# Kernel optimization log

Measured on AMD Instinct MI355X. Metric: run time of the kernel, lower is better.

Reference implementation:

```python
import jax, jax.numpy as jnp
import numpy as np

EPS = 1e-5
NEG_SLOPE = 0.2


def _minmax(a):
    m = jnp.min(a)
    return (a - m) / (jnp.max(a) - m)


def _bn(x2d, gamma, beta):
    # train-mode BatchNorm1d: stats over axis 0 (biased variance)
    mu = x2d.mean(0)
    var = x2d.var(0)
    return gamma * (x2d - mu) * jax.lax.rsqrt(var + EPS) + beta


def _leaky(a):
    return jnp.where(a >= 0, a, NEG_SLOPE * a)


def setup_inputs() -> dict:
    key = jax.random.key(0)
    ks = jax.random.split(key, 10)
    B, C, N = 256, 1024, 80
    stdv = 1.0 / np.sqrt(C)
    return {
        "x": jax.random.normal(ks[0], (B, C, N), jnp.float32),
        "out1": jax.random.normal(ks[1], (B, N), jnp.float32),
        "adj_param": jax.random.uniform(ks[2], (N, N), jnp.float32),
        "static_weight": jax.random.uniform(ks[3], (C, C), jnp.float32, -stdv, stdv),
        "dynamic_weight": jax.random.uniform(ks[4], (C, C), jnp.float32, -stdv, stdv),
        "conv_global_w": jax.random.normal(ks[5], (C, C), jnp.float32) * 0.02,
        "conv_global_b": jnp.zeros((C,), jnp.float32),
        "conv_co_w": jax.random.normal(ks[6], (N, 2 * C), jnp.float32) * 0.02,
        "conv_co_b": jnp.zeros((N,), jnp.float32),
        "bn_gamma": jnp.ones((C,), jnp.float32),
        "bn_beta": jnp.zeros((C,), jnp.float32),
        "bng_gamma": jnp.ones((C,), jnp.float32),
        "bng_beta": jnp.zeros((C,), jnp.float32),
    }


def reference(x, out1, adj_param, static_weight, dynamic_weight,
              conv_global_w, conv_global_b, conv_co_w, conv_co_b,
              bn_gamma, bn_beta, bng_gamma, bng_beta):
    B, C, N = x.shape

    # ---- static GCN ----
    sadj = _minmax(adj_param)                               # (N,N)
    D = jax.lax.rsqrt(sadj.sum(1))                          # A.sum(1)^-0.5
    adj = D[:, None] * sadj.T * D[None, :]                  # gen_adj, diag matmuls as broadcast
    support = jnp.einsum('bcn,co->bno', x, static_weight)   # (B,N,C)
    h = jnp.einsum('nm,bmo->bno', adj, support)             # (B,N,C)
    h = _bn(h.reshape(-1, C), bn_gamma, bn_beta).reshape(B, N, C)
    out_static = _leaky(h).transpose(0, 2, 1)               # (B,C,N)
    x2 = x + out_static

    # ---- dynamic graph construction ----
    glb = x2.mean(2)                                        # GAP over nodes -> (B,C)
    glb = glb @ conv_global_w.T + conv_global_b             # 1x1 conv
    glb = _leaky(_bn(glb, bng_gamma, bng_beta))             # BN over batch (L=1)
    cat = jnp.concatenate([jnp.broadcast_to(glb[:, :, None], (B, C, N)), x2], axis=1)  # (B,2C,N)
    dadj = jnp.einsum('oc,bcn->bon', conv_co_w, cat) + conv_co_b[None, :, None]        # (B,N,N)
    dadj = _minmax(dadj)

    # ---- adjacency loss ----
    t1 = jnp.einsum('bn,bnm->bm', out1, dadj) / N
    loss = jnp.sum(jnp.linalg.norm(out1 - t1, axis=1))
    loss = loss + jnp.sum(jnp.linalg.norm((dadj - sadj).reshape(B, -1), axis=1))

    # ---- dynamic GCN ----
    Dd = jax.lax.rsqrt(dadj.sum(2))                         # (B,N)
    tadj = Dd[:, :, None] * dadj.transpose(0, 2, 1) * Dd[:, None, :]
    sup = jnp.einsum('bcn,co->bno', x2, dynamic_weight)
    h2 = jnp.einsum('bnm,bmo->bno', tadj, sup)
    h2 = _bn(h2.reshape(-1, C), bn_gamma, bn_beta).reshape(B, N, C).transpose(0, 2, 1)
    h2 = _leaky(h2)                                         # (B,C,N)
    return h2, loss
```

## Files before the change

kernel.cpp:

```cpp
#include <hip/hip_runtime.h>
#include <hip/hip_bf16.h>
#include <math.h>

#define TPB 256

constexpr int   B_  = 256;
constexpr int   C_  = 1024;
constexpr int   N_  = 80;
constexpr int   BNr = B_ * N_;
constexpr int   CN  = C_ * N_;
constexpr long  BCN = (long)B_ * C_ * N_;
constexpr int   NN  = N_ * N_;
constexpr int   BNN = B_ * NN;
constexpr float EPSf = 1e-5f;

typedef __bf16 bf16x8 __attribute__((ext_vector_type(8)));
typedef float  f32x4  __attribute__((ext_vector_type(4)));

__device__ __forceinline__ float leakyf(float v) { return v >= 0.0f ? v : 0.2f * v; }

__device__ __forceinline__ ushort f2bf(float f) {
  __hip_bfloat16 h = __float2bfloat16(f);
  ushort u; __builtin_memcpy(&u, &h, 2); return u;
}
__device__ __forceinline__ float b2f(ushort u) {
  __hip_bfloat16 h; __builtin_memcpy(&h, &u, 2);
  return __bfloat162float(h);
}

#define GLOBAL_AS __attribute__((address_space(1)))
#define LDS_AS    __attribute__((address_space(3)))
__device__ __forceinline__ void load_lds16(const void* g, void* l) {
  __builtin_amdgcn_global_load_lds((const GLOBAL_AS void*)g, (LDS_AS void*)l, 16, 0, 0);
}

__global__ __launch_bounds__(256) void k_prep_all(
    const float* __restrict__ Ws, const float* __restrict__ Wd,
    const float* __restrict__ Wco, const float* __restrict__ Wg,
    ushort* __restrict__ Wts, ushort* __restrict__ Wtd,
    ushort* __restrict__ Wco1t, ushort* __restrict__ Wco2t, ushort* __restrict__ Wg_bf,
    float* __restrict__ zbase,
    const float* __restrict__ ap, float* __restrict__ sadj,
    ushort* __restrict__ adj_bf, float* __restrict__ lossa) {
  __shared__ float sh[NN];
  __shared__ float red[TPB];
  __shared__ float sD[N_];
  __shared__ float s_lo, s_hi;
  const int t = threadIdx.x;
  const int blk = blockIdx.x;
  if (blk < 2048) {
    const float* W = (blk < 1024) ? Ws : Wd;
    ushort* Wt = (blk < 1024) ? Wts : Wtd;
    const int bb = blk & 1023;
    const int bx = bb & 31, by = bb >> 5;
    const int tx = t % 32, ty = t / 32;
    const int r0 = by * 32, c0 = bx * 32;
#pragma unroll
    for (int k = 0; k < 4; ++k) sh[(ty + 8 * k) * 33 + tx] = W[(size_t)(r0 + ty + 8 * k) * C_ + c0 + tx];
    __syncthreads();
#pragma unroll
    for (int k = 0; k < 4; ++k) Wt[(size_t)(c0 + ty + 8 * k) * C_ + r0 + tx] = f2bf(sh[tx * 33 + ty + 8 * k]);
  } else if (blk < 2208) {
    const int i4 = ((blk - 2048) * TPB + t) * 4;
    const int o = i4 >> 11, k = i4 & 2047;
    float4 v = *(const float4*)&Wco[(size_t)o * 2048 + k];
    ushort4 u;
    u.x = f2bf(v.x); u.y = f2bf(v.y); u.z = f2bf(v.z); u.w = f2bf(v.w);
    if (k < C_) *(ushort4*)&Wco1t[(size_t)o * C_ + k] = u;
    else        *(ushort4*)&Wco2t[(size_t)o * C_ + (k - C_)] = u;
  } else if (blk < 3232) {
    const long i4 = ((long)(blk - 2208) * TPB + t) * 4;
    float4 v = *(const float4*)&Wg[i4];
    ushort4 u;
    u.x = f2bf(v.x); u.y = f2bf(v.y); u.z = f2bf(v.z); u.w = f2bf(v.w);
    *(ushort4*)&Wg_bf[i4] = u;
  } else if (blk < 3256) {
    const int i = ((blk - 3232) * TPB + t) * 4;
    float4 z = make_float4(0.f, 0.f, 0.f, 0.f);
    *(float4*)&zbase[i] = z;
  } else {
    float lo = 3.4e38f, hi = -3.4e38f;
    for (int i = t; i < NN; i += TPB) { float v = ap[i]; sh[i] = v; lo = fminf(lo, v); hi = fmaxf(hi, v); }
    red[t] = lo; __syncthreads();
    for (int o = 128; o > 0; o >>= 1) { if (t < o) red[t] = fminf(red[t], red[t + o]); __syncthreads(); }
    if (t == 0) s_lo = red[0];
    __syncthreads();
    red[t] = hi; __syncthreads();
    for (int o = 128; o > 0; o >>= 1) { if (t < o) red[t] = fmaxf(red[t], red[t + o]); __syncthreads(); }
    if (t == 0) s_hi = red[0];
    __syncthreads();
    const float inv = 1.0f / (s_hi - s_lo);
    for (int i = t; i < NN; i += TPB) { float v = (sh[i] - s_lo) * inv; sh[i] = v; sadj[i] = v; }
    __syncthreads();
    if (t < N_) { float sum = 0.f; for (int m = 0; m < N_; ++m) sum += sh[t * N_ + m]; sD[t] = rsqrtf(sum); }
    if (t == 0) *lossa = 0.0f;
    __syncthreads();
    for (int i = t; i < N_ * 96; i += TPB) {
      const int n = i / 96, m = i % 96;
      adj_bf[i] = f2bf((m < N_) ? sD[n] * sh[m * N_ + n] * sD[m] : 0.0f);
    }
  }
}

__global__ __launch_bounds__(256) void k_fold_mfma(const float* __restrict__ Xf32,
                                                   const ushort* __restrict__ Xbf,
                                                   const void* __restrict__ adjsrc,
                                                   ushort* __restrict__ outp, int mode,
                                                   const float* __restrict__ dmm) {
  __shared__ __align__(16) ushort sX[128][104];
  __shared__ __align__(16) ushort sAdj[80][104];
  __shared__ float sD[N_];
  const int t = threadIdx.x;
  const int b  = blockIdx.x >> 3;
  const int c0 = (blockIdx.x & 7) * 128;

  if (mode == 0) {
    const ushort* ab = (const ushort*)adjsrc;
    for (int i = t; i < (N_ * 96) / 4; i += TPB) {
      ushort4 v = *(const ushort4*)&ab[i * 4];
      *(ushort4*)&sAdj[(i * 4) / 96][(i * 4) % 96] = v;
    }
    __syncthreads();
  } else {
    float* sF = (float*)&sX[0][0];
    const float* db = (const float*)adjsrc + (size_t)b * NN;
    const float lo = dmm[0], inv = dmm[1];
    for (int i = t; i < NN / 4; i += TPB) {
      float4 v = *(const float4*)&db[i * 4];
      v.x = (v.x - lo) * inv; v.y = (v.y - lo) * inv;
      v.z = (v.z - lo) * inv; v.w = (v.w - lo) * inv;
      *(float4*)&sF[i * 4] = v;
    }
    __syncthreads();
    if (t < N_) { float s = 0.f; for (int m = 0; m < N_; ++m) s += sF[t * N_ + m]; sD[t] = rsqrtf(s); }
    __syncthreads();
    for (int i = t; i < N_ * 96; i += TPB) {
      const int n = i / 96, m = i % 96;
      sAdj[n][m] = f2bf((m < N_) ? sF[m * N_ + n] * sD[n] * sD[m] : 0.0f);
    }
    __syncthreads();
  }

  if (mode == 0) {
    const float* Xb = Xf32 + ((size_t)b * C_ + c0) * N_;
    for (int i = t; i < (128 * N_) / 4; i += TPB) {
      float4 v = *(const float4*)&Xb[i * 4];
      const int r = (i * 4) / N_, m = (i * 4) % N_;
      ushort4 u; u.x = f2bf(v.x); u.y = f2bf(v.y); u.z = f2bf(v.z); u.w = f2bf(v.w);
      *(ushort4*)&sX[r][m] = u;
    }
  } else {
    const ushort* Xb = Xbf + ((size_t)b * C_ + c0) * N_;
    for (int i = t; i < (128 * N_) / 8; i += TPB) {
      const int r = i / 10, m = (i % 10) * 8;
      uint4 v = *(const uint4*)&Xb[(size_t)r * N_ + m];
      *(uint4*)&sX[r][m] = v;
    }
  }
  for (int i = t; i < (128 * 16) / 4; i += TPB) {
    const int r = i / 4, m = 80 + (i % 4) * 4;
    ushort4 z; z.x = 0; z.y = 0; z.z = 0; z.w = 0;
    *(ushort4*)&sX[r][m] = z;
  }
  __syncthreads();

  const int lane = t & 63, wid = t >> 6;
  const int l16 = lane & 15, lq = lane >> 4;
  f32x4 acc[2][5];
#pragma unroll
  for (int i = 0; i < 2; ++i)
#pragma unroll
    for (int j = 0; j < 5; ++j) { f32x4 z = {0.f, 0.f, 0.f, 0.f}; acc[i][j] = z; }
  bf16x8 af[2][3], bfr[5][3];
#pragma unroll
  for (int i = 0; i < 2; ++i)
#pragma unroll
    for (int kk = 0; kk < 3; ++kk)
      af[i][kk] = *(const bf16x8*)&sX[wid * 32 + i * 16 + l16][kk * 32 + lq * 8];
#pragma unroll
  for (int j = 0; j < 5; ++j)
#pragma unroll
    for (int kk = 0; kk < 3; ++kk)
      bfr[j][kk] = *(const bf16x8*)&sAdj[j * 16 + l16][kk * 32 + lq * 8];
#pragma unroll
  for (int i = 0; i < 2; ++i)
#pragma unroll
    for (int j = 0; j < 5; ++j)
#pragma unroll
      for (int kk = 0; kk < 3; ++kk)
        acc[i][j] = __builtin_amdgcn_mfma_f32_16x16x32_bf16(af[i][kk], bfr[j][kk], acc[i][j], 0, 0, 0);

  ushort* ob = outp + (size_t)b * CN;
#pragma unroll
  for (int i = 0; i < 2; ++i) {
    const int c = c0 + wid * 32 + i * 16 + lq * 4;
#pragma unroll
    for (int j = 0; j < 5; ++j) {
      const int n = j * 16 + l16;
      ushort4 u;
      u.x = f2bf(acc[i][j][0]); u.y = f2bf(acc[i][j][1]);
      u.z = f2bf(acc[i][j][2]); u.w = f2bf(acc[i][j][3]);
      *(ushort4*)&ob[(size_t)n * C_ + c] = u;
    }
  }
}

__global__ __launch_bounds__(512, 2) void k_gemm_256(const ushort* __restrict__ A,
                                                     const ushort* __restrict__ Bt,
                                                     void* __restrict__ outp, int out_bf,
                                                     float* __restrict__ bnsum,
                                                     float* __restrict__ bnsq) {
  __shared__ ushort sA[2][256 * 64];
  __shared__ ushort sB[2][256 * 64];
  const int t = threadIdx.x;
  const int lane = t & 63, wid = t >> 6;
  const int wm = wid >> 2, wn = wid & 3;
  const int l16 = lane & 15, lq = lane >> 4;

  const int lin = blockIdx.x;
  const int xcd = lin & 7, bi = lin >> 3;
  const int tm = xcd * 10 + (bi >> 2);
  const int tn = bi & 3;
  const int m0 = tm * 256, o0 = tn * 256;

  const int srow = t >> 3;
  const int sswz = ((t & 7) ^ ((t >> 3) & 7)) * 8;

  f32x4 acc[8][4];
#pragma unroll
  for (int i = 0; i < 8; ++i)
#pragma unroll
    for (int j = 0; j < 4; ++j) { f32x4 z = {0.f, 0.f, 0.f, 0.f}; acc[i][j] = z; }

  bf16x8 afr[4][2], bfr0[2][2], bfr1[2][2];

#define STA(PAR, ROWB, KT) load_lds16(A  + (size_t)(m0 + (ROWB) + srow) * C_ + (KT) * 64 + sswz, \
                                      &sA[PAR][((ROWB) + (wid << 3)) * 64])
#define STB(PAR, ROWB, KT) load_lds16(Bt + (size_t)(o0 + (ROWB) + srow) * C_ + (KT) * 64 + sswz, \
                                      &sB[PAR][((ROWB) + (wid << 3)) * 64])
#define STA_H(PAR, H, KT) { STA(PAR, (H)*128, KT); STA(PAR, (H)*128 + 64, KT); }
#define STB_H(PAR, H, KT) { STB(PAR, (H)*128, KT); STB(PAR, (H)*128 + 64, KT); }

#define RDA(PAR, MH)                                                                      \
  _Pragma("unroll") for (int fi = 0; fi < 4; ++fi) {                                      \
    const int row = ((MH) ? 128 : 0) + wm * 64 + fi * 16 + l16;                           \
    _Pragma("unroll") for (int kk = 0; kk < 2; ++kk)                                      \
      afr[fi][kk] = *(const bf16x8*)&sA[PAR][row * 64 + ((kk * 4 + lq) ^ (l16 & 7)) * 8]; \
  }
#define RDB(PAR, NH, DST)                                                                 \
  _Pragma("unroll") for (int gi = 0; gi < 2; ++gi) {                                      \
    const int row = ((NH) ? 128 : 0) + wn * 32 + gi * 16 + l16;                           \
    _Pragma("unroll") for (int kk = 0; kk < 2; ++kk)                                      \
      DST[gi][kk] = *(const bf16x8*)&sB[PAR][row * 64 + ((kk * 4 + lq) ^ (l16 & 7)) * 8]; \
  }

#define MFMAS(MH, NH, BF)                                                          \
  _Pragma("unroll") for (int kk = 0; kk < 2; ++kk)                                 \
  _Pragma("unroll") for (int fi = 0; fi < 4; ++fi)                                 \
  _Pragma("unroll") for (int gi = 0; gi < 2; ++gi)                                 \
    acc[(MH) * 4 + fi][(NH) * 2 + gi] = __builtin_amdgcn_mfma_f32_16x16x32_bf16(   \
        afr[fi][kk], BF[gi][kk], acc[(MH) * 4 + fi][(NH) * 2 + gi], 0, 0, 0);

#define PHASE(MH, NH, BF, RD, STAGES, VMW)                                         \
  {                                                                                \
    RD                                                                             \
    STAGES                                                                         \
    asm volatile("s_barrier" ::: "memory");                                        \
    asm volatile("s_waitcnt lgkmcnt(0)" ::: "memory");                             \
    __builtin_amdgcn_s_setprio(1);                                                 \
    MFMAS(MH, NH, BF)                                                              \
    __builtin_amdgcn_s_setprio(0);                                                 \
    VMW                                                                            \
    asm volatile("s_barrier" ::: "memory");                                        \
  }

  STA_H(0, 0, 0); STA_H(0, 1, 0); STB_H(0, 0, 0); STB_H(0, 1, 0);
  STA_H(1, 0, 1); STB_H(1, 1, 1);
  asm volatile("s_waitcnt vmcnt(4)" ::: "memory");
  asm volatile("s_barrier" ::: "memory");

  for (int i = 0; i < 7; ++i) {
    const int t1 = 2 * i + 1, t2 = 2 * i + 2, t3 = 2 * i + 3;
    PHASE(0, 0, bfr0, RDA(0, 0) RDB(0, 0, bfr0), { STA_H(1, 1, t1); }, {})
    PHASE(0, 1, bfr1, RDB(0, 1, bfr1),           { STB_H(1, 0, t1); }, {})
    PHASE(1, 1, bfr1, RDA(0, 1),                 { STA_H(0, 0, t2); }, {})
    PHASE(1, 0, bfr0, {},                        { STB_H(0, 1, t2); }, { asm volatile("s_waitcnt vmcnt(4)" ::: "memory"); })
    PHASE(0, 0, bfr0, RDA(1, 0) RDB(1, 0, bfr0), { STA_H(0, 1, t2); }, {})
    PHASE(0, 1, bfr1, RDB(1, 1, bfr1),           { STB_H(0, 0, t2); }, {})
    PHASE(1, 1, bfr1, RDA(1, 1),                 { STA_H(1, 0, t3); }, {})
    PHASE(1, 0, bfr0, {},                        { STB_H(1, 1, t3); }, { asm volatile("s_waitcnt vmcnt(4)" ::: "memory"); })
  }
  PHASE(0, 0, bfr0, RDA(0, 0) RDB(0, 0, bfr0), { STA_H(1, 1, 15); }, {})
  PHASE(0, 1, bfr1, RDB(0, 1, bfr1),           { STB_H(1, 0, 15); }, {})
  PHASE(1, 1, bfr1, RDA(0, 1),                 {}, {})
  PHASE(1, 0, bfr0, {},                        {}, { asm volatile("s_waitcnt vmcnt(0)" ::: "memory"); })
  PHASE(0, 0, bfr0, RDA(1, 0) RDB(1, 0, bfr0), {}, {})
  PHASE(0, 1, bfr1, RDB(1, 1, bfr1),           {}, {})
  PHASE(1, 1, bfr1, RDA(1, 1),                 {}, {})
  PHASE(1, 0, bfr0, {},                        {}, {})

#pragma unroll
  for (int f = 0; f < 8; ++f) {
    const int gmb = (f < 4) ? (wm * 64 + f * 16) : (128 + wm * 64 + (f - 4) * 16);
    const int mg = m0 + gmb + lq * 4;
    const int b  = mg / 80;
    const int n0 = mg - b * 80;
#pragma unroll
    for (int gi = 0; gi < 4; ++gi) {
      const int gnb = (gi < 2) ? (wn * 32 + gi * 16) : (128 + wn * 32 + (gi - 2) * 16);
      const int og = o0 + gnb + l16;
      const size_t off = (size_t)b * CN + (size_t)og * N_ + n0;
      if (out_bf) {
        ushort4 u;
        u.x = f2bf(acc[f][gi][0]); u.y = f2bf(acc[f][gi][1]);
        u.z = f2bf(acc[f][gi][2]); u.w = f2bf(acc[f][gi][3]);
        *(ushort4*)((ushort*)outp + off) = u;
      } else {
        *(f32x4*)((float*)outp + off) = acc[f][gi];
      }
    }
  }

  {
    float* redS = (float*)&sA[0][0];
    float* redQ = redS + 2048;
    const int slot = wm * 4 + lq;
#pragma unroll
    for (int gi = 0; gi < 4; ++gi) {
      float s = 0.f, q = 0.f;
#pragma unroll
      for (int f = 0; f < 8; ++f)
#pragma unroll
        for (int r = 0; r < 4; ++r) { const float v = acc[f][gi][r]; s += v; q += v * v; }
      const int gnb = (gi < 2) ? (wn * 32 + gi * 16) : (128 + wn * 32 + (gi - 2) * 16);
      const int ol = gnb + l16;
      redS[ol * 8 + slot] = s;
      redQ[ol * 8 + slot] = q;
    }
    __syncthreads();
    if (t < 256) {
      float s = 0.f, q = 0.f;
#pragma unroll
      for (int k = 0; k < 8; ++k) { s += redS[t * 8 + k]; q += redQ[t * 8 + k]; }
      atomicAdd(&bnsum[o0 + t], s);
      atomicAdd(&bnsq[o0 + t], q);
    }
  }
#undef STA
#undef STB
#undef STA_H
#undef STB_H
#undef RDA
#undef RDB
#undef MFMAS
#undef PHASE
}

__global__ __launch_bounds__(256) void k_dadj_mfma(const ushort* __restrict__ A,
                                                   const ushort* __restrict__ Bw,
                                                   const float* __restrict__ go,
                                                   const float* __restrict__ bco,
                                                   float* __restrict__ dadj,
                                                   float* __restrict__ bmin,
                                                   float* __restrict__ bmax) {
  __shared__ ushort smA[128 * 32];
  __shared__ ushort smB[80 * 32];
  const int t = threadIdx.x;
  const int lane = t & 63, wid = t >> 6;
  const int m0 = blockIdx.x * 128;
  const int rto = t >> 2, ch = t & 3;
  const size_t gA0 = (size_t)(m0 + rto) * C_ + (size_t)ch * 8;
  ushort* ldsA = smA + wid * 512;
  const int l16 = lane & 15, lq = lane >> 4;
  const int wrow = wid * 32;
  f32x4 zero = {0.f, 0.f, 0.f, 0.f};
  f32x4 acc[2][5];
#pragma unroll
  for (int i = 0; i < 2; ++i)
#pragma unroll
    for (int j = 0; j < 5; ++j) acc[i][j] = zero;
  for (int k0 = 0; k0 < C_; k0 += 32) {
    load_lds16(A + gA0 + k0,            ldsA);
    load_lds16(A + gA0 + 64 * C_ + k0,  ldsA + 2048);
    {
      const int idx = t;
      uint4 v = *(const uint4*)&Bw[(size_t)(idx >> 2) * C_ + k0 + (idx & 3) * 8];
      *(uint4*)&smB[idx * 8] = v;
      if (t < 64) {
        const int idx2 = 256 + t;
        uint4 v2 = *(const uint4*)&Bw[(size_t)(idx2 >> 2) * C_ + k0 + (idx2 & 3) * 8];
        *(uint4*)&smB[idx2 * 8] = v2;
      }
    }
    __syncthreads();
    bf16x8 af[2], bfr[5];
#pragma unroll
    for (int i = 0; i < 2; ++i) af[i]  = *(const bf16x8*)&smA[(wrow + i * 16 + l16) * 32 + lq * 8];
#pragma unroll
    for (int j = 0; j < 5; ++j) bfr[j] = *(const bf16x8*)&smB[(j * 16 + l16) * 32 + lq * 8];
#pragma unroll
    for (int i = 0; i < 2; ++i)
#pragma unroll
      for (int j = 0; j < 5; ++j)
        acc[i][j] = __builtin_amdgcn_mfma_f32_16x16x32_bf16(af[i], bfr[j], acc[i][j], 0, 0, 0);
    __syncthreads();
  }
  float vlo = 3.4e38f, vhi = -3.4e38f;
#pragma unroll
  for (int i = 0; i < 2; ++i) {
    const int mg = m0 + wrow + i * 16 + lq * 4;
    const int b  = mg / 80;
    const int n0 = mg - b * 80;
    const float* gob = go + b * N_;
#pragma unroll
    for (int j = 0; j < 5; ++j) {
      const int o = j * 16 + l16;
      const float g = gob[o] + bco[o];
      f32x4 v = acc[i][j];
      v[0] += g; v[1] += g; v[2] += g; v[3] += g;
      vlo = fminf(vlo, fminf(fminf(v[0], v[1]), fminf(v[2], v[3])));
      vhi = fmaxf(vhi, fmaxf(fmaxf(v[0], v[1]), fmaxf(v[2], v[3])));
      *(f32x4*)&dadj[(size_t)b * NN + (size_t)o * N_ + n0] = v;
    }
  }
  float* red = (float*)smA;
  red[t] = vlo; red[TPB + t] = vhi;
  __syncthreads();
  for (int o = 128; o > 0; o >>= 1) {
    if (t < o) {
      red[t] = fminf(red[t], red[t + o]);
      red[TPB + t] = fmaxf(red[TPB + t], red[TPB + t + o]);
    }
    __syncthreads();
  }
  if (t == 0) { bmin[blockIdx.x] = red[0]; bmax[blockIdx.x] = red[TPB]; }
}

__global__ __launch_bounds__(256) void k_glb_mfma(const ushort* __restrict__ A,
                                                  const ushort* __restrict__ Bw,
                                                  const float* __restrict__ bias,
                                                  float* __restrict__ outp) {
  __shared__ ushort smA[2][64 * 32];
  __shared__ ushort smB[2][64 * 32];
  const int t = threadIdx.x;
  const int lane = t & 63, wid = t >> 6;
  const int o0 = blockIdx.x * 64, m0 = blockIdx.y * 64;
  const int rto = t >> 2, ch = t & 3;
  const size_t gA0 = (size_t)(m0 + rto) * C_ + (size_t)ch * 8;
  const size_t gB0 = (size_t)(o0 + rto) * C_ + (size_t)ch * 8;
  const int l16 = lane & 15, lq = lane >> 4;
  const int wm = wid & 1, wn = wid >> 1;
  f32x4 zero = {0.f, 0.f, 0.f, 0.f};
  f32x4 acc[2][2];
#pragma unroll
  for (int i = 0; i < 2; ++i)
#pragma unroll
    for (int j = 0; j < 2; ++j) acc[i][j] = zero;
  for (int k0 = 0; k0 < C_; k0 += 64) {
    load_lds16(A  + gA0 + k0,       smA[0] + wid * 512);
    load_lds16(A  + gA0 + k0 + 32,  smA[1] + wid * 512);
    load_lds16(Bw + gB0 + k0,       smB[0] + wid * 512);
    load_lds16(Bw + gB0 + k0 + 32,  smB[1] + wid * 512);
    __syncthreads();
#pragma unroll
    for (int h = 0; h < 2; ++h) {
      bf16x8 af[2], bfr[2];
#pragma unroll
      for (int i = 0; i < 2; ++i) af[i]  = *(const bf16x8*)&smA[h][(wm * 32 + i * 16 + l16) * 32 + lq * 8];
#pragma unroll
      for (int j = 0; j < 2; ++j) bfr[j] = *(const bf16x8*)&smB[h][(wn * 32 + j * 16 + l16) * 32 + lq * 8];
#pragma unroll
      for (int i = 0; i < 2; ++i)
#pragma unroll
        for (int j = 0; j < 2; ++j)
          acc[i][j] = __builtin_amdgcn_mfma_f32_16x16x32_bf16(af[i], bfr[j], acc[i][j], 0, 0, 0);
    }
    __syncthreads();
  }
#pragma unroll
  for (int i = 0; i < 2; ++i) {
    const int mg = m0 + wm * 32 + i * 16 + lq * 4;
#pragma unroll
    for (int j = 0; j < 2; ++j) {
      const int og = o0 + wn * 32 + j * 16 + l16;
      const float bs = bias[og];
      f32x4 v = acc[i][j];
#pragma unroll
      for (int r = 0; r < 4; ++r) outp[(size_t)(mg + r) * C_ + og] = v[r] + bs;
    }
  }
}

__global__ __launch_bounds__(256) void k_go_mfma(const ushort* __restrict__ A,
                                                 const ushort* __restrict__ Bw,
                                                 float* __restrict__ go) {
  __shared__ ushort smA[128 * 32];
  __shared__ ushort smB[80 * 32];
  const int t = threadIdx.x;
  const int lane = t & 63, wid = t >> 6;
  const int kbase = blockIdx.x * 128;
  const int m0 = blockIdx.y * 128;
  const int rto = t >> 2, ch = t & 3;
  const size_t gA0 = (size_t)(m0 + rto) * C_ + (size_t)ch * 8;
  ushort* ldsA = smA + wid * 512;
  const int l16 = lane & 15, lq = lane >> 4;
  const int wrow = wid * 32;
  f32x4 zero = {0.f, 0.f, 0.f, 0.f};
  f32x4 acc[2][5];
#pragma unroll
  for (int i = 0; i < 2; ++i)
#pragma unroll
    for (int j = 0; j < 5; ++j) acc[i][j] = zero;
  for (int kk0 = 0; kk0 < 128; kk0 += 32) {
    const int k0 = kbase + kk0;
    load_lds16(A + gA0 + k0,            ldsA);
    load_lds16(A + gA0 + 64 * C_ + k0,  ldsA + 2048);
    {
      const int idx = t;
      uint4 v = *(const uint4*)&Bw[(size_t)(idx >> 2) * C_ + k0 + (idx & 3) * 8];
      *(uint4*)&smB[idx * 8] = v;
      if (t < 64) {
        const int idx2 = 256 + t;
        uint4 v2 = *(const uint4*)&Bw[(size_t)(idx2 >> 2) * C_ + k0 + (idx2 & 3) * 8];
        *(uint4*)&smB[idx2 * 8] = v2;
      }
    }
    __syncthreads();
    bf16x8 af[2], bfr[5];
#pragma unroll
    for (int i = 0; i < 2; ++i) af[i]  = *(const bf16x8*)&smA[(wrow + i * 16 + l16) * 32 + lq * 8];
#pragma unroll
    for (int j = 0; j < 5; ++j) bfr[j] = *(const bf16x8*)&smB[(j * 16 + l16) * 32 + lq * 8];
#pragma unroll
    for (int i = 0; i < 2; ++i)
#pragma unroll
      for (int j = 0; j < 5; ++j)
        acc[i][j] = __builtin_amdgcn_mfma_f32_16x16x32_bf16(af[i], bfr[j], acc[i][j], 0, 0, 0);
    __syncthreads();
  }
#pragma unroll
  for (int i = 0; i < 2; ++i) {
    const int mg = m0 + wrow + i * 16 + lq * 4;
#pragma unroll
    for (int j = 0; j < 5; ++j) {
      const int o = j * 16 + l16;
#pragma unroll
      for (int r = 0; r < 4; ++r)
        atomicAdd(&go[(size_t)(mg + r) * N_ + o], acc[i][j][r]);
    }
  }
}

__global__ __launch_bounds__(256) void k_x2_fused(
    const float* __restrict__ x, ushort* __restrict__ hx,
    const float* __restrict__ g, const float* __restrict__ be,
    const float* __restrict__ ssum, const float* __restrict__ ssq,
    ushort* __restrict__ x2t, ushort* __restrict__ glb0b) {
  __shared__ float s[64][84];
  __shared__ float pg[64], pm[64], pb[64];
  const int t = threadIdx.x;
  const long row0 = (long)blockIdx.x * 64;
  const int b = (int)(row0 >> 10), c0 = (int)(row0 & 1023);
  if (t < 64) {
    const int c = c0 + t;
    const float mu = ssum[c] * (1.0f / BNr);
    const float var = ssq[c] * (1.0f / BNr) - mu * mu;
    const float rstd = rsqrtf(var + EPSf);
    pg[t] = g[c] * rstd; pm[t] = mu; pb[t] = be[c];
  }
  __syncthreads();
  const float* xb = x  + row0 * N_;
  ushort*      hb = hx + row0 * N_;
  for (int i4 = t; i4 < (64 * N_) / 4; i4 += TPB) {
    const int e = i4 * 4, r = e / N_, n = e % N_;
    float4 xv = *(const float4*)&xb[e];
    ushort4 hu = *(const ushort4*)&hb[e];
    const float gm = pg[r], m = pm[r], bb = pb[r];
    float4 o;
    o.x = xv.x + leakyf(gm * (b2f(hu.x) - m) + bb);
    o.y = xv.y + leakyf(gm * (b2f(hu.y) - m) + bb);
    o.z = xv.z + leakyf(gm * (b2f(hu.z) - m) + bb);
    o.w = xv.w + leakyf(gm * (b2f(hu.w) - m) + bb);
    *(float4*)&s[r][n] = o;
    ushort4 ou;
    ou.x = f2bf(o.x); ou.y = f2bf(o.y); ou.z = f2bf(o.z); ou.w = f2bf(o.w);
    *(ushort4*)&hb[e] = ou;
  }
  __syncthreads();
  const int tx = t % 16, ty = t / 16;
  ushort* tb = x2t + (size_t)b * CN + c0 + tx * 4;
#pragma unroll
  for (int u = 0; u < 5; ++u) {
    const int n = ty + 16 * u;
    ushort4 v;
    v.x = f2bf(s[tx * 4 + 0][n]); v.y = f2bf(s[tx * 4 + 1][n]);
    v.z = f2bf(s[tx * 4 + 2][n]); v.w = f2bf(s[tx * 4 + 3][n]);
    *(ushort4*)&tb[(size_t)n * C_] = v;
  }
  {
    const int r = t >> 2, q = t & 3;
    float sacc = 0.f;
    for (int n = q; n < N_; n += 4) sacc += s[r][n];
    sacc += __shfl_down(sacc, 1);
    sacc += __shfl_down(sacc, 2);
    if (q == 0) glb0b[(size_t)b * C_ + c0 + r] = f2bf(sacc * (1.0f / N_));
  }
}

__global__ void k_bng(const float* __restrict__ glb1, const float* __restrict__ gg,
                      const float* __restrict__ gb, ushort* __restrict__ glbf) {
  const int c = blockIdx.x, t = threadIdx.x;
  const float v = glb1[(long)t * C_ + c];
  __shared__ float rs[TPB], rq[TPB];
  rs[t] = v; rq[t] = v * v; __syncthreads();
  for (int o = 128; o > 0; o >>= 1) { if (t < o) { rs[t] += rs[t + o]; rq[t] += rq[t + o]; } __syncthreads(); }
  __shared__ float sm, sr;
  if (t == 0) { const float m = rs[0] / B_; const float var = rq[0] / B_ - m * m; sm = m; sr = rsqrtf(var + EPSf); }
  __syncthreads();
  glbf[(long)t * C_ + c] = f2bf(leakyf(gg[c] * (v - sm) * sr + gb[c]));
}

__global__ void k_minmax2(const float* __restrict__ bmin, const float* __restrict__ bmax, float* __restrict__ dmm) {
  const int t = threadIdx.x;
  float lo = (t < 160) ? bmin[t] : 3.4e38f;
  float hi = (t < 160) ? bmax[t] : -3.4e38f;
  __shared__ float rl[TPB], rh[TPB];
  rl[t] = lo; rh[t] = hi; __syncthreads();
  for (int o = 128; o > 0; o >>= 1) { if (t < o) { rl[t] = fminf(rl[t], rl[t + o]); rh[t] = fmaxf(rh[t], rh[t + o]); } __syncthreads(); }
  if (t == 0) { dmm[0] = rl[0]; dmm[1] = 1.0f / (rh[0] - rl[0]); }
}

__global__ void k_loss(const float* __restrict__ dadj, const float* __restrict__ sadj,
                       const float* __restrict__ out1, float* __restrict__ lossa,
                       const float* __restrict__ dmm) {
  const int b = blockIdx.x, t = threadIdx.x;
  const float* db = dadj + (long)b * NN;
  const float* o1 = out1 + b * N_;
  const float lo = dmm[0], inv = dmm[1];
  float p2 = 0.f;
  for (int i = t; i < NN; i += TPB) { const float d = (db[i] - lo) * inv - sadj[i]; p2 += d * d; }
  float p1 = 0.f;
  if (t < N_) {
    float acc = 0.f;
    for (int n = 0; n < N_; ++n) acc += o1[n] * ((db[n * N_ + t] - lo) * inv);
    const float d = o1[t] - acc * (1.0f / N_);
    p1 = d * d;
  }
  __shared__ float red[TPB];
  __shared__ float s2;
  red[t] = p2; __syncthreads();
  for (int o = 128; o > 0; o >>= 1) { if (t < o) red[t] += red[t + o]; __syncthreads(); }
  if (t == 0) s2 = red[0];
  __syncthreads();
  red[t] = p1; __syncthreads();
  for (int o = 128; o > 0; o >>= 1) { if (t < o) red[t] += red[t + o]; __syncthreads(); }
  if (t == 0) atomicAdd(lossa, sqrtf(s2) + sqrtf(red[0]));
}

__global__ void k_final(const ushort* __restrict__ h2, float* __restrict__ outp,
                        const float* __restrict__ g, const float* __restrict__ be,
                        const float* __restrict__ ssum, const float* __restrict__ ssq,
                        const float* __restrict__ lossa) {
  const long i = ((long)blockIdx.x * TPB + threadIdx.x) * 4;
  const int c = (int)((i / N_) % C_);
  ushort4 hu = *(const ushort4*)&h2[i];
  const float mu = ssum[c] * (1.0f / BNr);
  const float rstd = rsqrtf(ssq[c] * (1.0f / BNr) - mu * mu + EPSf);
  const float gm = g[c] * rstd, bb = be[c];
  float4 v;
  v.x = leakyf(gm * (b2f(hu.x) - mu) + bb);
  v.y = leakyf(gm * (b2f(hu.y) - mu) + bb);
  v.z = leakyf(gm * (b2f(hu.z) - mu) + bb);
  v.w = leakyf(gm * (b2f(hu.w) - mu) + bb);
  *(float4*)&outp[i] = v;
  if (blockIdx.x == 0 && threadIdx.x == 0) outp[BCN] = *lossa;
}

extern "C" void kernel_launch(void* const* d_in, const int* in_sizes, int n_in,
                              void* d_out, int out_size, void* d_ws, size_t ws_size,
                              hipStream_t stream) {
  const float* x    = (const float*)d_in[0];
  const float* out1 = (const float*)d_in[1];
  const float* ap   = (const float*)d_in[2];
  const float* Ws   = (const float*)d_in[3];
  const float* Wd   = (const float*)d_in[4];
  const float* Wg   = (const float*)d_in[5];
  const float* bg   = (const float*)d_in[6];
  const float* Wco  = (const float*)d_in[7];
  const float* bco  = (const float*)d_in[8];
  const float* bn_g  = (const float*)d_in[9];
  const float* bn_b  = (const float*)d_in[10];
  const float* bng_g = (const float*)d_in[11];
  const float* bng_b = (const float*)d_in[12];
  float* out = (float*)d_out;

  float* w = (float*)d_ws;
  float* sadj  = w;
  float* dadj  = sadj + NN;
  float* glb0  = dadj + BNN;
  float* glb1  = glb0 + B_ * C_;
  float* glbf  = glb1 + B_ * C_;
  float* go    = glbf + B_ * C_;
  float* ssum1 = go + BNr;
  float* ssq1  = ssum1 + C_;
  float* ssum2 = ssq1 + C_;
  float* ssq2  = ssum2 + C_;
  float* bmin  = ssq2 + C_;
  float* bmax  = bmin + 512;
  float* dmm   = bmax + 512;
  float* lossa = dmm + 2;
  ushort* ub   = (ushort*)(((uintptr_t)(lossa + 1) + 255) & ~(uintptr_t)255);
  ushort* xa_bf  = ub;
  ushort* hT_bf  = xa_bf + BCN;
  ushort* Wts    = hT_bf + BCN;
  ushort* Wtd    = Wts + (size_t)C_ * C_;
  ushort* Wco2t  = Wtd + (size_t)C_ * C_;
  ushort* adj_bf = Wco2t + (size_t)N_ * C_;
  ushort* Wg_bf   = (ushort*)dadj;
  ushort* Wco1t   = (ushort*)dadj + (size_t)C_ * C_;
  ushort* glb0_bf = (ushort*)glb0;
  ushort* glbf_bf = (ushort*)glbf;
  ushort* x2t_bf  = xa_bf;

  k_prep_all<<<3257, TPB, 0, stream>>>(Ws, Wd, Wco, Wg, Wts, Wtd, Wco1t, Wco2t, Wg_bf,
                                       go, ap, sadj, adj_bf, lossa);

  k_fold_mfma<<<B_ * 8, TPB, 0, stream>>>(x, hT_bf, adj_bf, xa_bf, 0, dmm);
  k_gemm_256<<<320, 512, 0, stream>>>(xa_bf, Wts, hT_bf, 1, ssum1, ssq1);
  k_x2_fused<<<(B_ * C_) / 64, TPB, 0, stream>>>(x, hT_bf, bn_g, bn_b, ssum1, ssq1,
                                                 x2t_bf, glb0_bf);

  k_glb_mfma<<<dim3(C_ / 64, B_ / 64), TPB, 0, stream>>>(glb0_bf, Wg_bf, bg, glb1);
  k_bng<<<C_, TPB, 0, stream>>>(glb1, bng_g, bng_b, glbf_bf);
  k_go_mfma<<<dim3(8, B_ / 128), TPB, 0, stream>>>(glbf_bf, Wco1t, go);
  k_dadj_mfma<<<BNr / 128, TPB, 0, stream>>>(x2t_bf, Wco2t, go, bco, dadj, bmin, bmax);
  k_minmax2<<<1, TPB, 0, stream>>>(bmin, bmax, dmm);

  k_loss<<<B_, TPB, 0, stream>>>(dadj, sadj, out1, lossa, dmm);

  k_fold_mfma<<<B_ * 8, TPB, 0, stream>>>(x, hT_bf, dadj, xa_bf, 1, dmm);
  k_gemm_256<<<320, 512, 0, stream>>>(xa_bf, Wtd, hT_bf, 1, ssum2, ssq2);
  k_final<<<(int)(BCN / (4 * TPB)), TPB, 0, stream>>>(hT_bf, out, bn_g, bn_b, ssum2, ssq2, lossa);
}
```

Before: 503.4 us.

## Fuse BN-global stats into glb GEMM and fold minmax reduction into consumers

The global-branch BatchNorm statistics are now accumulated with atomics in the epilogue of the glb GEMM, and the normalize, leaky and bf16 conversion is applied while the go GEMM loads its A operand. This removes the separate k_bng kernel and the glbf buffer. The single-block min/max kernel is also removed: k_loss and k_fold_mfma each reduce the 160 per-block partials themselves. Two launches and a round trip through global memory go away, at the cost of redundant small reductions in every consumer block and atomics on two more zeroed buffers.

```diff
diff --git a/kernel.cpp b/kernel.cpp
--- a/kernel.cpp
+++ b/kernel.cpp
@@ -74,7 +74,7 @@
     ushort4 u;
     u.x = f2bf(v.x); u.y = f2bf(v.y); u.z = f2bf(v.z); u.w = f2bf(v.w);
     *(ushort4*)&Wg_bf[i4] = u;
-  } else if (blk < 3256) {
+  } else if (blk < 3258) {
     const int i = ((blk - 3232) * TPB + t) * 4;
     float4 z = make_float4(0.f, 0.f, 0.f, 0.f);
     *(float4*)&zbase[i] = z;
@@ -106,10 +106,13 @@
                                                    const ushort* __restrict__ Xbf,
                                                    const void* __restrict__ adjsrc,
                                                    ushort* __restrict__ outp, int mode,
-                                                   const float* __restrict__ dmm) {
+                                                   const float* __restrict__ bmin,
+                                                   const float* __restrict__ bmax) {
   __shared__ __align__(16) ushort sX[128][104];
   __shared__ __align__(16) ushort sAdj[80][104];
   __shared__ float sD[N_];
+  __shared__ float rl[TPB], rh[TPB];
+  __shared__ float s_lo, s_inv;
   const int t = threadIdx.x;
   const int b  = blockIdx.x >> 3;
   const int c0 = (blockIdx.x & 7) * 128;
@@ -122,9 +125,18 @@
     }
     __syncthreads();
   } else {
+    rl[t] = (t < 160) ? bmin[t] : 3.4e38f;
+    rh[t] = (t < 160) ? bmax[t] : -3.4e38f;
+    __syncthreads();
+    for (int o = 128; o > 0; o >>= 1) {
+      if (t < o) { rl[t] = fminf(rl[t], rl[t + o]); rh[t] = fmaxf(rh[t], rh[t + o]); }
+      __syncthreads();
+    }
+    if (t == 0) { s_lo = rl[0]; s_inv = 1.0f / (rh[0] - rl[0]); }
+    __syncthreads();
+    const float lo = s_lo, inv = s_inv;
     float* sF = (float*)&sX[0][0];
     const float* db = (const float*)adjsrc + (size_t)b * NN;
-    const float lo = dmm[0], inv = dmm[1];
     for (int i = t; i < NN / 4; i += TPB) {
       float4 v = *(const float4*)&db[i * 4];
       v.x = (v.x - lo) * inv; v.y = (v.y - lo) * inv;
@@ -439,7 +451,9 @@
 __global__ __launch_bounds__(256) void k_glb_mfma(const ushort* __restrict__ A,
                                                   const ushort* __restrict__ Bw,
                                                   const float* __restrict__ bias,
-                                                  float* __restrict__ outp) {
+                                                  float* __restrict__ outp,
+                                                  float* __restrict__ gsum,
+                                                  float* __restrict__ gsq) {
   __shared__ ushort smA[2][64 * 32];
   __shared__ ushort smB[2][64 * 32];
   const int t = threadIdx.x;
@@ -477,6 +491,7 @@
     }
     __syncthreads();
   }
+  float ssv[2] = {0.f, 0.f}, sqv[2] = {0.f, 0.f};
 #pragma unroll
   for (int i = 0; i < 2; ++i) {
     const int mg = m0 + wm * 32 + i * 16 + lq * 4;
@@ -486,25 +501,57 @@
       const float bs = bias[og];
       f32x4 v = acc[i][j];
 #pragma unroll
-      for (int r = 0; r < 4; ++r) outp[(size_t)(mg + r) * C_ + og] = v[r] + bs;
-    }
-  }
-}
-
-__global__ __launch_bounds__(256) void k_go_mfma(const ushort* __restrict__ A,
+      for (int r = 0; r < 4; ++r) {
+        const float val = v[r] + bs;
+        outp[(size_t)(mg + r) * C_ + og] = val;
+        ssv[j] += val; sqv[j] += val * val;
+      }
+    }
+  }
+  {
+    float* redS = (float*)&smA[0][0];
+    float* redQ = redS + 512;
+    const int slot = wm * 4 + lq;
+#pragma unroll
+    for (int j = 0; j < 2; ++j) {
+      const int ol = wn * 32 + j * 16 + l16;
+      redS[ol * 8 + slot] = ssv[j];
+      redQ[ol * 8 + slot] = sqv[j];
+    }
+    __syncthreads();
+    if (t < 64) {
+      float s = 0.f, q = 0.f;
+#pragma unroll
+      for (int k = 0; k < 8; ++k) { s += redS[t * 8 + k]; q += redQ[t * 8 + k]; }
+      atomicAdd(&gsum[o0 + t], s);
+      atomicAdd(&gsq[o0 + t], q);
+    }
+  }
+}
+
+__global__ __launch_bounds__(256) void k_go_mfma(const float* __restrict__ glb1,
                                                  const ushort* __restrict__ Bw,
+                                                 const float* __restrict__ gsum,
+                                                 const float* __restrict__ gsq,
+                                                 const float* __restrict__ gg,
+                                                 const float* __restrict__ gb,
                                                  float* __restrict__ go) {
   __shared__ ushort smA[128 * 32];
   __shared__ ushort smB[80 * 32];
+  __shared__ float pgm[C_], pmu[C_], pgb[C_];
   const int t = threadIdx.x;
   const int lane = t & 63, wid = t >> 6;
   const int kbase = blockIdx.x * 128;
   const int m0 = blockIdx.y * 128;
   const int rto = t >> 2, ch = t & 3;
-  const size_t gA0 = (size_t)(m0 + rto) * C_ + (size_t)ch * 8;
-  ushort* ldsA = smA + wid * 512;
   const int l16 = lane & 15, lq = lane >> 4;
   const int wrow = wid * 32;
+  for (int c = t; c < C_; c += TPB) {
+    const float mu = gsum[c] * (1.0f / B_);
+    const float var = gsq[c] * (1.0f / B_) - mu * mu;
+    pgm[c] = gg[c] * rsqrtf(var + EPSf); pmu[c] = mu; pgb[c] = gb[c];
+  }
+  __syncthreads();
   f32x4 zero = {0.f, 0.f, 0.f, 0.f};
   f32x4 acc[2][5];
 #pragma unroll
@@ -513,8 +560,25 @@
     for (int j = 0; j < 5; ++j) acc[i][j] = zero;
   for (int kk0 = 0; kk0 < 128; kk0 += 32) {
     const int k0 = kbase + kk0;
-    load_lds16(A + gA0 + k0,            ldsA);
-    load_lds16(A + gA0 + 64 * C_ + k0,  ldsA + 2048);
+#pragma unroll
+    for (int h = 0; h < 2; ++h) {
+      const float* src = &glb1[(size_t)(m0 + h * 64 + rto) * C_ + k0 + ch * 8];
+      float4 a0 = *(const float4*)src;
+      float4 a1 = *(const float4*)(src + 4);
+      float av[8] = {a0.x, a0.y, a0.z, a0.w, a1.x, a1.y, a1.z, a1.w};
+      ushort4 u0, u1;
+      const int cb = k0 + ch * 8;
+      u0.x = f2bf(leakyf(pgm[cb+0]*(av[0]-pmu[cb+0])+pgb[cb+0]));
+      u0.y = f2bf(leakyf(pgm[cb+1]*(av[1]-pmu[cb+1])+pgb[cb+1]));
+      u0.z = f2bf(leakyf(pgm[cb+2]*(av[2]-pmu[cb+2])+pgb[cb+2]));
+      u0.w = f2bf(leakyf(pgm[cb+3]*(av[3]-pmu[cb+3])+pgb[cb+3]));
+      u1.x = f2bf(leakyf(pgm[cb+4]*(av[4]-pmu[cb+4])+pgb[cb+4]));
+      u1.y = f2bf(leakyf(pgm[cb+5]*(av[5]-pmu[cb+5])+pgb[cb+5]));
+      u1.z = f2bf(leakyf(pgm[cb+6]*(av[6]-pmu[cb+6])+pgb[cb+6]));
+      u1.w = f2bf(leakyf(pgm[cb+7]*(av[7]-pmu[cb+7])+pgb[cb+7]));
+      *(ushort4*)&smA[h * 2048 + t * 8]     = u0;
+      *(ushort4*)&smA[h * 2048 + t * 8 + 4] = u1;
+    }
     {
       const int idx = t;
       uint4 v = *(const uint4*)&Bw[(size_t)(idx >> 2) * C_ + k0 + (idx & 3) * 8];
@@ -556,7 +620,7 @@
     const float* __restrict__ g, const float* __restrict__ be,
     const float* __restrict__ ssum, const float* __restrict__ ssq,
     ushort* __restrict__ x2t, ushort* __restrict__ glb0b) {
-  __shared__ float s[64][84];
+  __shared__ float s[64][85];
   __shared__ float pg[64], pm[64], pb[64];
   const int t = threadIdx.x;
   const long row0 = (long)blockIdx.x * 64;
@@ -607,36 +671,24 @@
   }
 }
 
-__global__ void k_bng(const float* __restrict__ glb1, const float* __restrict__ gg,
-                      const float* __restrict__ gb, ushort* __restrict__ glbf) {
-  const int c = blockIdx.x, t = threadIdx.x;
-  const float v = glb1[(long)t * C_ + c];
-  __shared__ float rs[TPB], rq[TPB];
-  rs[t] = v; rq[t] = v * v; __syncthreads();
-  for (int o = 128; o > 0; o >>= 1) { if (t < o) { rs[t] += rs[t + o]; rq[t] += rq[t + o]; } __syncthreads(); }
-  __shared__ float sm, sr;
-  if (t == 0) { const float m = rs[0] / B_; const float var = rq[0] / B_ - m * m; sm = m; sr = rsqrtf(var + EPSf); }
-  __syncthreads();
-  glbf[(long)t * C_ + c] = f2bf(leakyf(gg[c] * (v - sm) * sr + gb[c]));
-}
-
-__global__ void k_minmax2(const float* __restrict__ bmin, const float* __restrict__ bmax, float* __restrict__ dmm) {
-  const int t = threadIdx.x;
-  float lo = (t < 160) ? bmin[t] : 3.4e38f;
-  float hi = (t < 160) ? bmax[t] : -3.4e38f;
-  __shared__ float rl[TPB], rh[TPB];
-  rl[t] = lo; rh[t] = hi; __syncthreads();
-  for (int o = 128; o > 0; o >>= 1) { if (t < o) { rl[t] = fminf(rl[t], rl[t + o]); rh[t] = fmaxf(rh[t], rh[t + o]); } __syncthreads(); }
-  if (t == 0) { dmm[0] = rl[0]; dmm[1] = 1.0f / (rh[0] - rl[0]); }
-}
-
 __global__ void k_loss(const float* __restrict__ dadj, const float* __restrict__ sadj,
                        const float* __restrict__ out1, float* __restrict__ lossa,
-                       const float* __restrict__ dmm) {
+                       const float* __restrict__ bmin, const float* __restrict__ bmax) {
   const int b = blockIdx.x, t = threadIdx.x;
+  __shared__ float red[TPB], red2[TPB];
+  __shared__ float slo, sinv, s2;
+  red[t]  = (t < 160) ? bmin[t] : 3.4e38f;
+  red2[t] = (t < 160) ? bmax[t] : -3.4e38f;
+  __syncthreads();
+  for (int o = 128; o > 0; o >>= 1) {
+    if (t < o) { red[t] = fminf(red[t], red[t + o]); red2[t] = fmaxf(red2[t], red2[t + o]); }
+    __syncthreads();
+  }
+  if (t == 0) { slo = red[0]; sinv = 1.0f / (red2[0] - red[0]); }
+  __syncthreads();
+  const float lo = slo, inv = sinv;
   const float* db = dadj + (long)b * NN;
   const float* o1 = out1 + b * N_;
-  const float lo = dmm[0], inv = dmm[1];
   float p2 = 0.f;
   for (int i = t; i < NN; i += TPB) { const float d = (db[i] - lo) * inv - sadj[i]; p2 += d * d; }
   float p1 = 0.f;
@@ -646,8 +698,6 @@
     const float d = o1[t] - acc * (1.0f / N_);
     p1 = d * d;
   }
-  __shared__ float red[TPB];
-  __shared__ float s2;
   red[t] = p2; __syncthreads();
   for (int o = 128; o > 0; o >>= 1) { if (t < o) red[t] += red[t + o]; __syncthreads(); }
   if (t == 0) s2 = red[0];
@@ -699,16 +749,16 @@
   float* dadj  = sadj + NN;
   float* glb0  = dadj + BNN;
   float* glb1  = glb0 + B_ * C_;
-  float* glbf  = glb1 + B_ * C_;
-  float* go    = glbf + B_ * C_;
+  float* go    = glb1 + B_ * C_;
   float* ssum1 = go + BNr;
   float* ssq1  = ssum1 + C_;
   float* ssum2 = ssq1 + C_;
   float* ssq2  = ssum2 + C_;
-  float* bmin  = ssq2 + C_;
+  float* gsum  = ssq2 + C_;
+  float* gsq   = gsum + C_;
+  float* bmin  = gsq + C_;
   float* bmax  = bmin + 512;
-  float* dmm   = bmax + 512;
-  float* lossa = dmm + 2;
+  float* lossa = bmax + 512;
   ushort* ub   = (ushort*)(((uintptr_t)(lossa + 1) + 255) & ~(uintptr_t)255);
   ushort* xa_bf  = ub;
   ushort* hT_bf  = xa_bf + BCN;
@@ -719,26 +769,23 @@
   ushort* Wg_bf   = (ushort*)dadj;
   ushort* Wco1t   = (ushort*)dadj + (size_t)C_ * C_;
   ushort* glb0_bf = (ushort*)glb0;
-  ushort* glbf_bf = (ushort*)glbf;
   ushort* x2t_bf  = xa_bf;
 
-  k_prep_all<<<3257, TPB, 0, stream>>>(Ws, Wd, Wco, Wg, Wts, Wtd, Wco1t, Wco2t, Wg_bf,
+  k_prep_all<<<3259, TPB, 0, stream>>>(Ws, Wd, Wco, Wg, Wts, Wtd, Wco1t, Wco2t, Wg_bf,
                                        go, ap, sadj, adj_bf, lossa);
 
-  k_fold_mfma<<<B_ * 8, TPB, 0, stream>>>(x, hT_bf, adj_bf, xa_bf, 0, dmm);
+  k_fold_mfma<<<B_ * 8, TPB, 0, stream>>>(x, hT_bf, adj_bf, xa_bf, 0, bmin, bmax);
   k_gemm_256<<<320, 512, 0, stream>>>(xa_bf, Wts, hT_bf, 1, ssum1, ssq1);
   k_x2_fused<<<(B_ * C_) / 64, TPB, 0, stream>>>(x, hT_bf, bn_g, bn_b, ssum1, ssq1,
                                                  x2t_bf, glb0_bf);
 
-  k_glb_mfma<<<dim3(C_ / 64, B_ / 64), TPB, 0, stream>>>(glb0_bf, Wg_bf, bg, glb1);
-  k_bng<<<C_, TPB, 0, stream>>>(glb1, bng_g, bng_b, glbf_bf);
-  k_go_mfma<<<dim3(8, B_ / 128), TPB, 0, stream>>>(glbf_bf, Wco1t, go);
+  k_glb_mfma<<<dim3(C_ / 64, B_ / 64), TPB, 0, stream>>>(glb0_bf, Wg_bf, bg, glb1, gsum, gsq);
+  k_go_mfma<<<dim3(8, B_ / 128), TPB, 0, stream>>>(glb1, Wco1t, gsum, gsq, bng_g, bng_b, go);
   k_dadj_mfma<<<BNr / 128, TPB, 0, stream>>>(x2t_bf, Wco2t, go, bco, dadj, bmin, bmax);
-  k_minmax2<<<1, TPB, 0, stream>>>(bmin, bmax, dmm);
-
-  k_loss<<<B_, TPB, 0, stream>>>(dadj, sadj, out1, lossa, dmm);
-
-  k_fold_mfma<<<B_ * 8, TPB, 0, stream>>>(x, hT_bf, dadj, xa_bf, 1, dmm);
+
+  k_loss<<<B_, TPB, 0, stream>>>(dadj, sadj, out1, lossa, bmin, bmax);
+
+  k_fold_mfma<<<B_ * 8, TPB, 0, stream>>>(x, hT_bf, dadj, xa_bf, 1, bmin, bmax);
   k_gemm_256<<<320, 512, 0, stream>>>(xa_bf, Wtd, hT_bf, 1, ssum2, ssq2);
   k_final<<<(int)(BCN / (4 * TPB)), TPB, 0, stream>>>(hT_bf, out, bn_g, bn_b, ssum2, ssq2, lossa);
 }
```

After: 501.2 us. Within noise of the previous version (-0.4%).
